# Kernel optimization log

Hardware: AMD Instinct MI355X
Metric: run time of the kernel (lower is better)

## Reference

```python
import jax, jax.numpy as jnp
import numpy as np

B, N, P = 8, 4096, 1024
P4 = P // 4
EPS = 1e-5


def _ln(x, g, b):
    mu = jnp.mean(x, axis=-1, keepdims=True)
    var = jnp.var(x, axis=-1, keepdims=True)
    return (x - mu) * jax.lax.rsqrt(var + EPS) * g + b


def setup_inputs() -> dict:
    key = jax.random.key(0)
    ks = jax.random.split(key, 16)
    s = lambda fan: 1.0 / np.sqrt(fan)
    return {
        "xyz": jax.random.normal(ks[0], (B, N, 3), jnp.float32),
        "x": jax.random.normal(ks[1], (B, N, P), jnp.float32),
        "ln1_g": jnp.ones((P,), jnp.float32),
        "ln1_b": jnp.zeros((P,), jnp.float32),
        "ln2_g": jnp.ones((P,), jnp.float32),
        "ln2_b": jnp.zeros((P,), jnp.float32),
        "qk_w": jax.random.normal(ks[2], (P4, P), jnp.float32) * s(P),   # shared q/k 1x1 conv, no bias
        "v_w": jax.random.normal(ks[3], (P, P), jnp.float32) * s(P),
        "v_b": jax.random.normal(ks[4], (P,), jnp.float32) * s(P),
        "t1_w": jax.random.normal(ks[5], (P, P4), jnp.float32) * s(P4),  # trans_conv
        "t1_b": jax.random.normal(ks[6], (P,), jnp.float32) * s(P4),
        "t2_w": jax.random.normal(ks[7], (P, P4), jnp.float32) * s(P4),  # trans_conv1
        "t2_b": jax.random.normal(ks[8], (P,), jnp.float32) * s(P4),
        "m1_w": jax.random.normal(ks[9], (P, P), jnp.float32) * s(P),
        "m1_b": jax.random.normal(ks[10], (P,), jnp.float32) * s(P),
        "m2_w": jax.random.normal(ks[11], (P, P), jnp.float32) * s(P),
        "m2_b": jax.random.normal(ks[12], (P,), jnp.float32) * s(P),
    }


def reference(xyz, x, ln1_g, ln1_b, ln2_g, ln2_b, qk_w, v_w, v_b,
              t1_w, t1_b, t2_w, t2_b, m1_w, m1_b, m2_w, m2_b):
    # xyz is accepted but unused, matching the torch module. Dropout = eval identity.
    res1 = x
    h = _ln(x, ln1_g, ln1_b)                                   # [B,N,P]
    # TransformerBlock_1 (1x1 convs on h^T [B,P,N] are just matmuls over P)
    x_q = jnp.einsum('op,bnp->bon', qk_w, h)                   # [B,P4,N]
    # k shares weights with q; x_k permuted is x_q transposed
    x_v = jnp.einsum('op,bnp->bno', v_w, h) + v_b              # [B,N,P]
    energy = jnp.einsum('bqn,bkn->bqk', x_q, x_q)              # [B,P4,P4]
    att = jnp.einsum('op,bpk->bok', t1_w, energy) + t1_b[:, None]   # [B,P,P4]
    att = jax.nn.gelu(att, approximate=False)
    att = jnp.einsum('op,bkp->bok', t2_w, att) + t2_b[:, None]      # [B,P,P]
    att = jax.nn.softmax(att, axis=-1)
    t_out = jnp.einsum('bnp,bpq->bnq', x_v, att)               # [B,N,P]
    x1 = t_out + res1
    h2 = _ln(x1, ln2_g, ln2_b)
    m = jax.nn.gelu(h2 @ m1_w.T + m1_b, approximate=False)
    m = m @ m2_w.T + m2_b
    return x1 + m
```

## Files before the change

### kernel.cpp

```cpp
#include <hip/hip_runtime.h>


typedef __attribute__((ext_vector_type(4))) float f32x4;
typedef __attribute__((ext_vector_type(8))) _Float16 h16x8;
typedef __attribute__((ext_vector_type(8))) unsigned short u16x8;
typedef __attribute__((ext_vector_type(4))) unsigned short u16x4;

__device__ __forceinline__ unsigned short f2h(float f) {
  _Float16 h = (_Float16)f;
  return __builtin_bit_cast(unsigned short, h);
}
__device__ __forceinline__ float h2f(unsigned short u) {
  return (float)__builtin_bit_cast(_Float16, u);
}
__device__ __forceinline__ unsigned split16(float f) {
  _Float16 h = (_Float16)f;
  _Float16 l = (_Float16)(f - (float)h);
  return (unsigned)__builtin_bit_cast(unsigned short, h) |
         ((unsigned)__builtin_bit_cast(unsigned short, l) << 16);
}
__device__ __forceinline__ float gelu_f(float x) {
  return 0.5f * x * (1.0f + erff(x * 0.70710678118654752f));
}
__device__ __forceinline__ void gload16(const void* g, void* l) {
  __builtin_amdgcn_global_load_lds(
      (const __attribute__((address_space(1))) unsigned int*)g,
      (__attribute__((address_space(3))) unsigned int*)l, 16, 0, 0);
}
#define FENCE() asm volatile("" ::: "memory")

__device__ __forceinline__ void xcd_swz(int& bx, int& by, int gx, int gy) {
  const int nwg = gx * gy;
  if ((nwg & 7) == 0 && nwg >= 16) {
    const int flat = bx + gx * by;
    const int chunk = nwg >> 3;
    const int nf = (flat & 7) * chunk + (flat >> 3);
    bx = nf % gx;
    by = nf / gx;
  }
}

__global__ __launch_bounds__(256)
void ln_kernel(const float* __restrict__ x, const float* __restrict__ g,
               const float* __restrict__ b, unsigned short* __restrict__ hi,
               unsigned short* __restrict__ lo, unsigned short* __restrict__ xh) {
  __shared__ float red[16];
  const size_t base = (size_t)blockIdx.x * 1024;
  const int t = threadIdx.x;
  f32x4 v = *(const f32x4*)&x[base + t * 4];
  float s = v[0] + v[1] + v[2] + v[3];
  float q = v[0] * v[0] + v[1] * v[1] + v[2] * v[2] + v[3] * v[3];
#pragma unroll
  for (int o = 32; o > 0; o >>= 1) { s += __shfl_down(s, o); q += __shfl_down(q, o); }
  const int w = t >> 6;
  if ((t & 63) == 0) { red[w] = s; red[8 + w] = q; }
  __syncthreads();
  s = (red[0] + red[1]) + (red[2] + red[3]);
  q = (red[8] + red[9]) + (red[10] + red[11]);
  const float mu = s * (1.0f / 1024.0f);
  const float var = q * (1.0f / 1024.0f) - mu * mu;
  const float is = rsqrtf(var + 1e-5f);
  f32x4 gg = *(const f32x4*)&g[t * 4];
  f32x4 bb = *(const f32x4*)&b[t * 4];
  u16x4 oh, ol, ox;
#pragma unroll
  for (int j = 0; j < 4; j++) {
    float y = (v[j] - mu) * is * gg[j] + bb[j];
    unsigned p = split16(y);
    oh[j] = (unsigned short)(p & 0xffffu);
    ol[j] = (unsigned short)(p >> 16);
    ox[j] = f2h(v[j]);
  }
  *(u16x4*)&hi[base + t * 4] = oh;
  if (lo) *(u16x4*)&lo[base + t * 4] = ol;
  if (xh) *(u16x4*)&xh[base + t * 4] = ox;
}

__global__ __launch_bounds__(256)
void stats16_kernel(const unsigned short* __restrict__ x16, float* __restrict__ muis) {
  __shared__ float red[16];
  const size_t base = (size_t)blockIdx.x * 1024;
  const int t = threadIdx.x;
  u16x4 raw = *(const u16x4*)&x16[base + t * 4];
  float v[4];
#pragma unroll
  for (int j = 0; j < 4; j++) v[j] = h2f(raw[j]);
  float s = v[0] + v[1] + v[2] + v[3];
  float q = v[0] * v[0] + v[1] * v[1] + v[2] * v[2] + v[3] * v[3];
#pragma unroll
  for (int o = 32; o > 0; o >>= 1) { s += __shfl_down(s, o); q += __shfl_down(q, o); }
  const int w = t >> 6;
  if ((t & 63) == 0) { red[w] = s; red[8 + w] = q; }
  __syncthreads();
  if (t == 0) {
    s = (red[0] + red[1]) + (red[2] + red[3]);
    q = (red[8] + red[9]) + (red[10] + red[11]);
    const float mu = s * (1.0f / 1024.0f);
    const float var = q * (1.0f / 1024.0f) - mu * mu;
    muis[blockIdx.x * 2] = mu;
    muis[blockIdx.x * 2 + 1] = rsqrtf(var + 1e-5f);
  }
}

__global__ __launch_bounds__(256)
void cvt_kernel(const float* __restrict__ in, unsigned short* __restrict__ hi,
                unsigned short* __restrict__ lo, int n4) {
  int i = blockIdx.x * 256 + threadIdx.x;
  if (i < n4) {
    f32x4 v = *(const f32x4*)&in[(size_t)i * 4];
    u16x4 oh, ol;
#pragma unroll
    for (int j = 0; j < 4; j++) {
      unsigned p = split16(v[j]);
      oh[j] = (unsigned short)(p & 0xffffu);
      ol[j] = (unsigned short)(p >> 16);
    }
    *(u16x4*)&hi[(size_t)i * 4] = oh;
    if (lo) *(u16x4*)&lo[(size_t)i * 4] = ol;
  }
}

__global__ __launch_bounds__(256)
void vwt_kernel(const float* __restrict__ vw, unsigned short* __restrict__ wvt) {
  __shared__ float T[64][65];
  const int bx = blockIdx.x, by = blockIdx.y;
  const int t = threadIdx.x;
  const int lr = t >> 6, lc = t & 63;
#pragma unroll
  for (int i = 0; i < 16; ++i) {
    const int row = i * 4 + lr;
    T[row][lc] = vw[(size_t)(by * 64 + row) * 1024 + bx * 64 + lc];
  }
  __syncthreads();
#pragma unroll
  for (int i = 0; i < 16; ++i) {
    const int row = i * 4 + lr;
    wvt[(size_t)(bx * 64 + row) * 1024 + by * 64 + lc] = f2h(T[lc][row]);
  }
}

__global__ __launch_bounds__(256)
void beff_kernel(const unsigned short* __restrict__ attT, const float* __restrict__ vb,
                 float* __restrict__ beff) {
  const int b = blockIdx.y;
  const int q = blockIdx.x * 4 + (threadIdx.x >> 6);
  const int l = threadIdx.x & 63;
  const unsigned short* row = attT + ((size_t)b * 1024 + q) * 1024;
  float s = 0.0f;
#pragma unroll
  for (int i = 0; i < 2; ++i) {
    u16x8 v = *(const u16x8*)&row[(i * 64 + l) * 8];
    f32x4 vb0 = *(const f32x4*)&vb[(i * 64 + l) * 8];
    f32x4 vb1 = *(const f32x4*)&vb[(i * 64 + l) * 8 + 4];
#pragma unroll
    for (int j = 0; j < 4; j++) s += h2f(v[j]) * vb0[j];
#pragma unroll
    for (int j = 0; j < 4; j++) s += h2f(v[j + 4]) * vb1[j];
  }
#pragma unroll
  for (int o = 32; o > 0; o >>= 1) s += __shfl_down(s, o);
  if (l == 0) beff[b * 1024 + q] = s;
}

template <int EPI>
__global__ __launch_bounds__(256)
void gemm_v(const unsigned short* __restrict__ Ain, const unsigned short* __restrict__ Bin,
            void* __restrict__ Cout, const float* __restrict__ bias,
            const unsigned short* __restrict__ res16In,
            int K, int lda, int ldb, int ldc,
            long long sA, long long sB, long long sC, long long sBias, long long sRes) {
  __shared__ short As[2][4096];
  __shared__ short Bs[2][4096];
  const int z = blockIdx.z;
  const unsigned short* A = Ain + (size_t)z * sA;
  const unsigned short* B = Bin + (size_t)z * sB;
  int bx = blockIdx.x, by = blockIdx.y;
  xcd_swz(bx, by, gridDim.x, gridDim.y);
  const int mBase = by * 128, nBase = bx * 128;
  const int t = threadIdx.x, w = t >> 6, l = t & 63;
  const int r16 = l & 15, kq = l >> 4;
  const int wr = (w >> 1) * 64, wc = (w & 1) * 64;
  f32x4 acc[4][4] = {};

  auto stage = [&](int buf, int k0) {
#pragma unroll
    for (int i = 0; i < 2; ++i) {
      const int c = i * 256 + t;
      const int row = c >> 2, cc = c & 3;
      const int gc = cc ^ ((row >> 1) & 3);
      short* la = &As[buf][(i * 256 + w * 64) * 8];
      short* lb = &Bs[buf][(i * 256 + w * 64) * 8];
      gload16(&A[(size_t)(mBase + row) * lda + k0 + gc * 8], la);
      gload16(&B[(size_t)(nBase + row) * ldb + k0 + gc * 8], lb);
    }
  };

  const int nt = K >> 5;
  stage(0, 0);
  if (nt > 1) stage(1, 32);
  for (int ts = 0; ts < nt; ++ts) {
    const int cur = ts & 1;
    if (ts + 1 < nt) { asm volatile("s_waitcnt vmcnt(4)" ::: "memory"); }
    else             { asm volatile("s_waitcnt vmcnt(0)" ::: "memory"); }
    __builtin_amdgcn_s_barrier();
    FENCE();
    h16x8 aF[4], bF[4];
#pragma unroll
    for (int mi = 0; mi < 4; mi++) {
      const int r = wr + mi * 16 + r16;
      aF[mi] = *(const h16x8*)&As[cur][r * 32 + (kq ^ ((r >> 1) & 3)) * 8];
    }
#pragma unroll
    for (int ni = 0; ni < 4; ni++) {
      const int r = wc + ni * 16 + r16;
      bF[ni] = *(const h16x8*)&Bs[cur][r * 32 + (kq ^ ((r >> 1) & 3)) * 8];
    }
    __builtin_amdgcn_s_setprio(1);
#pragma unroll
    for (int mi = 0; mi < 4; mi++)
#pragma unroll
      for (int ni = 0; ni < 4; ni++)
        acc[mi][ni] = __builtin_amdgcn_mfma_f32_16x16x32_f16(aF[mi], bF[ni], acc[mi][ni], 0, 0, 0);
    __builtin_amdgcn_s_setprio(0);
    FENCE();
    __builtin_amdgcn_s_barrier();
    FENCE();
    if (ts + 2 < nt) stage(cur, (ts + 2) * 32);
  }
  FENCE();

  unsigned short* C16 = (unsigned short*)Cout + (size_t)z * sC;
  float* C32 = (float*)Cout + (size_t)z * sC;
  const float* bp = (EPI == 1 || EPI == 3 || EPI == 8) ? bias + (size_t)z * sBias : nullptr;
  const unsigned short* rp = (EPI == 3 || EPI == 8) ? res16In + (size_t)z * sRes : nullptr;

  if constexpr (EPI == 1 || EPI == 4 || EPI == 8) {
    short* ep = ((w & 2) ? &Bs[0][0] : &As[0][0]) + (w & 1) * 4096;
#pragma unroll
    for (int mi = 0; mi < 4; mi++) {
#pragma unroll
      for (int ni = 0; ni < 4; ni++) {
        const int cl = nBase + wc + ni * 16 + r16;
        const float bcol = bp ? bp[cl] : 0.0f;
#pragma unroll
        for (int r = 0; r < 4; r++) {
          float v = acc[mi][ni][r] + bcol;
          if (EPI == 1) v = gelu_f(v);
          ep[(mi * 16 + kq * 4 + r) * 64 + ni * 16 + r16] = (short)f2h(v);
        }
      }
    }
#pragma unroll
    for (int j = 0; j < 8; j++) {
      const int f = j * 512 + l * 8;
      const int row = f >> 6, col = f & 63;
      u16x8 v8 = *(const u16x8*)&ep[f];
      const size_t gi = (size_t)(mBase + wr + row) * ldc + nBase + wc + col;
      if (EPI == 8) {
        u16x8 r8 = *(const u16x8*)&rp[gi];
#pragma unroll
        for (int q = 0; q < 8; q++) v8[q] = f2h(h2f(v8[q]) + h2f(r8[q]));
      }
      *(u16x8*)&C16[gi] = v8;
    }
  } else {
#pragma unroll
    for (int mi = 0; mi < 4; mi++) {
#pragma unroll
      for (int ni = 0; ni < 4; ni++) {
        const int cl = nBase + wc + ni * 16 + r16;
        const float bcol = bp[cl];
#pragma unroll
        for (int r = 0; r < 4; r++) {
          const int rw = mBase + wr + mi * 16 + kq * 4 + r;
          const size_t idx = (size_t)rw * ldc + cl;
          C32[idx] = acc[mi][ni][r] + bcol + h2f(rp[idx]);
        }
      }
    }
  }
}

__global__ __launch_bounds__(256)
void gemm_r(const unsigned short* __restrict__ Ain, const unsigned short* __restrict__ Bin,
            unsigned short* __restrict__ Cout, const float* __restrict__ bias,
            const unsigned short* __restrict__ resIn,
            int K, int lda, int ldb, int ldc,
            long long sA, long long sB, long long sC, long long sBias, long long sRes) {
  __shared__ short As[2][4096];
  __shared__ short Bs[2][4096];
  const int z = blockIdx.z;
  const unsigned short* A = Ain + (size_t)z * sA;
  const unsigned short* B = Bin + (size_t)z * sB;
  int bx = blockIdx.x, by = blockIdx.y;
  xcd_swz(bx, by, gridDim.x, gridDim.y);
  const int mBase = by * 128, nBase = bx * 128;
  const int t = threadIdx.x, w = t >> 6, l = t & 63;
  const int r16 = l & 15, kq = l >> 4;
  const int wr = (w >> 1) * 64, wc = (w & 1) * 64;
  f32x4 acc[4][4] = {};

  const int row0 = t >> 2, row1 = 64 + (t >> 2);
  const int cc0 = t & 3;
  const int gc0 = cc0 ^ ((row0 >> 1) & 3);
  const int gc1 = cc0 ^ ((row1 >> 1) & 3);

  u16x8 ra0, ra1, rb0, rb1;
  auto loadreg = [&](int k0) {
    ra0 = *(const u16x8*)&A[(size_t)(mBase + row0) * lda + k0 + gc0 * 8];
    rb0 = *(const u16x8*)&B[(size_t)(nBase + row0) * ldb + k0 + gc0 * 8];
    ra1 = *(const u16x8*)&A[(size_t)(mBase + row1) * lda + k0 + gc1 * 8];
    rb1 = *(const u16x8*)&B[(size_t)(nBase + row1) * ldb + k0 + gc1 * 8];
  };
  auto dswrite = [&](int buf) {
    *(u16x8*)&As[buf][t * 8] = ra0;
    *(u16x8*)&Bs[buf][t * 8] = rb0;
    *(u16x8*)&As[buf][(256 + t) * 8] = ra1;
    *(u16x8*)&Bs[buf][(256 + t) * 8] = rb1;
  };

  const int nt = K >> 5;
  loadreg(0);
  dswrite(0);
  if (nt > 1) loadreg(32);
  asm volatile("s_waitcnt lgkmcnt(0)" ::: "memory");
  __builtin_amdgcn_s_barrier();
  FENCE();
  for (int ts = 0; ts < nt; ++ts) {
    const int cur = ts & 1;
    h16x8 aF[4], bF[4];
#pragma unroll
    for (int mi = 0; mi < 4; mi++) {
      const int r = wr + mi * 16 + r16;
      aF[mi] = *(const h16x8*)&As[cur][r * 32 + (kq ^ ((r >> 1) & 3)) * 8];
    }
#pragma unroll
    for (int ni = 0; ni < 4; ni++) {
      const int r = wc + ni * 16 + r16;
      bF[ni] = *(const h16x8*)&Bs[cur][r * 32 + (kq ^ ((r >> 1) & 3)) * 8];
    }
    __builtin_amdgcn_s_setprio(1);
#pragma unroll
    for (int mi = 0; mi < 4; mi++)
#pragma unroll
      for (int ni = 0; ni < 4; ni++)
        acc[mi][ni] = __builtin_amdgcn_mfma_f32_16x16x32_f16(aF[mi], bF[ni], acc[mi][ni], 0, 0, 0);
    __builtin_amdgcn_s_setprio(0);
    FENCE();
    if (ts + 1 < nt) {
      __builtin_amdgcn_s_barrier();
      FENCE();
      dswrite((ts + 1) & 1);
      if (ts + 2 < nt) loadreg((ts + 2) * 32);
      asm volatile("s_waitcnt lgkmcnt(0)" ::: "memory");
      FENCE();
      __builtin_amdgcn_s_barrier();
      FENCE();
    }
  }
  FENCE();

  unsigned short* C16 = Cout + (size_t)z * sC;
  const float* bp = bias + (size_t)z * sBias;
  const unsigned short* rp = resIn + (size_t)z * sRes;
  short* ep = ((w & 2) ? &Bs[0][0] : &As[0][0]) + (w & 1) * 4096;
#pragma unroll
  for (int mi = 0; mi < 4; mi++) {
#pragma unroll
    for (int ni = 0; ni < 4; ni++) {
      const int cl = nBase + wc + ni * 16 + r16;
      const float bcol = bp[cl];
#pragma unroll
      for (int r = 0; r < 4; r++)
        ep[(mi * 16 + kq * 4 + r) * 64 + ni * 16 + r16] =
            (short)f2h(acc[mi][ni][r] + bcol);
    }
  }
#pragma unroll
  for (int j = 0; j < 8; j++) {
    const int f = j * 512 + l * 8;
    const int row = f >> 6, col = f & 63;
    u16x8 v8 = *(const u16x8*)&ep[f];
    const size_t gi = (size_t)(mBase + wr + row) * ldc + nBase + wc + col;
    u16x8 r8 = *(const u16x8*)&rp[gi];
#pragma unroll
    for (int q = 0; q < 8; q++) v8[q] = f2h(h2f(v8[q]) + h2f(r8[q]));
    *(u16x8*)&C16[gi] = v8;
  }
}

__global__ __launch_bounds__(256)
void gemm_m(const unsigned short* __restrict__ Ain, const unsigned short* __restrict__ Bin,
            const float* __restrict__ muis, const float* __restrict__ lng,
            const float* __restrict__ lnb, const float* __restrict__ bias,
            unsigned short* __restrict__ Cout, int K, int lda, int ldb, int ldc) {
  __shared__ short As[2][4096];
  __shared__ short Bs[2][4096];
  int bx = blockIdx.x, by = blockIdx.y;
  xcd_swz(bx, by, gridDim.x, gridDim.y);
  const int mBase = by * 128, nBase = bx * 128;
  const int t = threadIdx.x, w = t >> 6, l = t & 63;
  const int r16 = l & 15, kq = l >> 4;
  const int wr = (w >> 1) * 64, wc = (w & 1) * 64;
  f32x4 acc[4][4] = {};

  const int row0 = t >> 2, row1 = 64 + (t >> 2);
  const int cc0 = t & 3;
  const int gc0 = cc0 ^ ((row0 >> 1) & 3);
  const int gc1 = cc0 ^ ((row1 >> 1) & 3);
  const float mu0 = muis[(mBase + row0) * 2], is0 = muis[(mBase + row0) * 2 + 1];
  const float mu1 = muis[(mBase + row1) * 2], is1 = muis[(mBase + row1) * 2 + 1];

  u16x8 ra0, ra1, rb0, rb1;
  auto loadreg = [&](int k0) {
    ra0 = *(const u16x8*)&Ain[(size_t)(mBase + row0) * lda + k0 + gc0 * 8];
    rb0 = *(const u16x8*)&Bin[(size_t)(nBase + row0) * ldb + k0 + gc0 * 8];
    ra1 = *(const u16x8*)&Ain[(size_t)(mBase + row1) * lda + k0 + gc1 * 8];
    rb1 = *(const u16x8*)&Bin[(size_t)(nBase + row1) * ldb + k0 + gc1 * 8];
  };
  auto dswrite = [&](int buf, int k0) {
    {
      const int cb = k0 + gc0 * 8;
      f32x4 g0 = *(const f32x4*)&lng[cb], g1 = *(const f32x4*)&lng[cb + 4];
      f32x4 b0 = *(const f32x4*)&lnb[cb], b1 = *(const f32x4*)&lnb[cb + 4];
      u16x8 o;
#pragma unroll
      for (int j = 0; j < 4; j++) o[j] = f2h((h2f(ra0[j]) - mu0) * is0 * g0[j] + b0[j]);
#pragma unroll
      for (int j = 0; j < 4; j++) o[j + 4] = f2h((h2f(ra0[j + 4]) - mu0) * is0 * g1[j] + b1[j]);
      *(u16x8*)&As[buf][t * 8] = o;
      *(u16x8*)&Bs[buf][t * 8] = rb0;
    }
    {
      const int cb = k0 + gc1 * 8;
      f32x4 g0 = *(const f32x4*)&lng[cb], g1 = *(const f32x4*)&lng[cb + 4];
      f32x4 b0 = *(const f32x4*)&lnb[cb], b1 = *(const f32x4*)&lnb[cb + 4];
      u16x8 o;
#pragma unroll
      for (int j = 0; j < 4; j++) o[j] = f2h((h2f(ra1[j]) - mu1) * is1 * g0[j] + b0[j]);
#pragma unroll
      for (int j = 0; j < 4; j++) o[j + 4] = f2h((h2f(ra1[j + 4]) - mu1) * is1 * g1[j] + b1[j]);
      *(u16x8*)&As[buf][(256 + t) * 8] = o;
      *(u16x8*)&Bs[buf][(256 + t) * 8] = rb1;
    }
  };

  const int nt = K >> 5;
  loadreg(0);
  dswrite(0, 0);
  if (nt > 1) loadreg(32);
  asm volatile("s_waitcnt lgkmcnt(0)" ::: "memory");
  __builtin_amdgcn_s_barrier();
  FENCE();
  for (int ts = 0; ts < nt; ++ts) {
    const int cur = ts & 1;
    h16x8 aF[4], bF[4];
#pragma unroll
    for (int mi = 0; mi < 4; mi++) {
      const int r = wr + mi * 16 + r16;
      aF[mi] = *(const h16x8*)&As[cur][r * 32 + (kq ^ ((r >> 1) & 3)) * 8];
    }
#pragma unroll
    for (int ni = 0; ni < 4; ni++) {
      const int r = wc + ni * 16 + r16;
      bF[ni] = *(const h16x8*)&Bs[cur][r * 32 + (kq ^ ((r >> 1) & 3)) * 8];
    }
    __builtin_amdgcn_s_setprio(1);
#pragma unroll
    for (int mi = 0; mi < 4; mi++)
#pragma unroll
      for (int ni = 0; ni < 4; ni++)
        acc[mi][ni] = __builtin_amdgcn_mfma_f32_16x16x32_f16(aF[mi], bF[ni], acc[mi][ni], 0, 0, 0);
    __builtin_amdgcn_s_setprio(0);
    FENCE();
    if (ts + 1 < nt) {
      __builtin_amdgcn_s_barrier();
      FENCE();
      dswrite((ts + 1) & 1, (ts + 1) * 32);
      if (ts + 2 < nt) loadreg((ts + 2) * 32);
      asm volatile("s_waitcnt lgkmcnt(0)" ::: "memory");
      FENCE();
      __builtin_amdgcn_s_barrier();
      FENCE();
    }
  }
  FENCE();

  short* ep = ((w & 2) ? &Bs[0][0] : &As[0][0]) + (w & 1) * 4096;
#pragma unroll
  for (int mi = 0; mi < 4; mi++) {
#pragma unroll
    for (int ni = 0; ni < 4; ni++) {
      const int cl = nBase + wc + ni * 16 + r16;
      const float bcol = bias[cl];
#pragma unroll
      for (int r = 0; r < 4; r++)
        ep[(mi * 16 + kq * 4 + r) * 64 + ni * 16 + r16] =
            (short)f2h(gelu_f(acc[mi][ni][r] + bcol));
    }
  }
#pragma unroll
  for (int j = 0; j < 8; j++) {
    const int f = j * 512 + l * 8;
    const int row = f >> 6, col = f & 63;
    *(u16x8*)&Cout[(size_t)(mBase + wr + row) * ldc + nBase + wc + col] =
        *(const u16x8*)&ep[f];
  }
}

template <int EPI, int SWAP>
__global__ __launch_bounds__(256)
void gemm_s(const unsigned short* __restrict__ Ahi, const unsigned short* __restrict__ Alo,
            const unsigned short* __restrict__ Bhi, const unsigned short* __restrict__ Blo,
            void* __restrict__ Cout, unsigned short* __restrict__ Cout2,
            const float* __restrict__ bias,
            int K, int lda, int ldb, int ldc,
            long long sA, long long sB, long long sC, int splitK) {
  __shared__ short As[2][8192];
  __shared__ short Bs[2][8192];
  const int z = blockIdx.z;
  const int bi = z / splitK, sp = z % splitK;
  const int kLen = K / splitK, kStart = sp * kLen;
  const unsigned short* AH = Ahi + (size_t)bi * sA;
  const unsigned short* BH = Bhi + (size_t)bi * sB;
  const unsigned short* AL = Alo + (size_t)bi * sA;
  const unsigned short* BL = Blo + (size_t)bi * sB;
  int bx = blockIdx.x, by = blockIdx.y;
  xcd_swz(bx, by, gridDim.x, gridDim.y);
  const int mBase = (SWAP ? bx : by) * 128, nBase = (SWAP ? by : bx) * 128;
  const int t = threadIdx.x, w = t >> 6, l = t & 63;
  const int r16 = l & 15, kq = l >> 4;
  const int wr = (w >> 1) * 64, wc = (w & 1) * 64;
  f32x4 acc[4][4] = {};

  auto stage = [&](int buf, int k0) {
#pragma unroll
    for (int i = 0; i < 2; ++i) {
      const int c = i * 256 + t;
      const int row = c >> 2, cc = c & 3;
      const int gc = cc ^ ((row >> 1) & 3);
      const int cbase = i * 256 + w * 64;
      const size_t ga = (size_t)(mBase + row) * lda + k0 + gc * 8;
      const size_t gb = (size_t)(nBase + row) * ldb + k0 + gc * 8;
      gload16(&AH[ga], &As[buf][cbase * 8]);
      gload16(&AL[ga], &As[buf][4096 + cbase * 8]);
      gload16(&BH[gb], &Bs[buf][cbase * 8]);
      gload16(&BL[gb], &Bs[buf][4096 + cbase * 8]);
    }
  };

  const int nsteps = kLen >> 5;
  stage(0, kStart);
  if (nsteps > 1) stage(1, kStart + 32);
  for (int ts = 0; ts < nsteps; ++ts) {
    const int cur = ts & 1;
    if (ts + 1 < nsteps) { asm volatile("s_waitcnt vmcnt(8)" ::: "memory"); }
    else                 { asm volatile("s_waitcnt vmcnt(0)" ::: "memory"); }
    __builtin_amdgcn_s_barrier();
    FENCE();
    h16x8 aH[4], bH[4], aL[4], bL[4];
#pragma unroll
    for (int mi = 0; mi < 4; mi++) {
      const int r = wr + mi * 16 + r16;
      const int off = r * 32 + (kq ^ ((r >> 1) & 3)) * 8;
      aH[mi] = *(const h16x8*)&As[cur][off];
      aL[mi] = *(const h16x8*)&As[cur][4096 + off];
    }
#pragma unroll
    for (int ni = 0; ni < 4; ni++) {
      const int r = wc + ni * 16 + r16;
      const int off = r * 32 + (kq ^ ((r >> 1) & 3)) * 8;
      bH[ni] = *(const h16x8*)&Bs[cur][off];
      bL[ni] = *(const h16x8*)&Bs[cur][4096 + off];
    }
    __builtin_amdgcn_s_setprio(1);
#pragma unroll
    for (int mi = 0; mi < 4; mi++)
#pragma unroll
      for (int ni = 0; ni < 4; ni++) {
        acc[mi][ni] = __builtin_amdgcn_mfma_f32_16x16x32_f16(aH[mi], bH[ni], acc[mi][ni], 0, 0, 0);
        acc[mi][ni] = __builtin_amdgcn_mfma_f32_16x16x32_f16(aH[mi], bL[ni], acc[mi][ni], 0, 0, 0);
        acc[mi][ni] = __builtin_amdgcn_mfma_f32_16x16x32_f16(aL[mi], bH[ni], acc[mi][ni], 0, 0, 0);
      }
    __builtin_amdgcn_s_setprio(0);
    FENCE();
    __builtin_amdgcn_s_barrier();
    FENCE();
    if (ts + 2 < nsteps) stage(cur, kStart + (ts + 2) * 32);
  }
  FENCE();

  unsigned short* C16 = (unsigned short*)Cout + (size_t)z * sC;
  unsigned short* C16b = Cout2 ? Cout2 + (size_t)z * sC : nullptr;
  float* C32 = (float*)Cout + (size_t)z * sC;

  if constexpr (EPI == 4 || EPI == 6) {
    short* ep = &As[0][0] + w * 4096;
    unsigned pk[4][4][4];
#pragma unroll
    for (int mi = 0; mi < 4; mi++)
#pragma unroll
      for (int ni = 0; ni < 4; ni++)
#pragma unroll
        for (int r = 0; r < 4; r++) {
          float v = acc[mi][ni][r];
          if (EPI == 6) { v += bias[mBase + wr + mi * 16 + kq * 4 + r]; v = gelu_f(v); }
          pk[mi][ni][r] = split16(v);
        }
#pragma unroll
    for (int mi = 0; mi < 4; mi++)
#pragma unroll
      for (int ni = 0; ni < 4; ni++)
#pragma unroll
        for (int r = 0; r < 4; r++)
          ep[(mi * 16 + kq * 4 + r) * 64 + ni * 16 + r16] =
              (short)(pk[mi][ni][r] & 0xffffu);
#pragma unroll
    for (int j = 0; j < 8; j++) {
      const int f = j * 512 + l * 8;
      const int row = f >> 6, col = f & 63;
      *(u16x8*)&C16[(size_t)(mBase + wr + row) * ldc + nBase + wc + col] =
          *(const u16x8*)&ep[f];
    }
#pragma unroll
    for (int mi = 0; mi < 4; mi++)
#pragma unroll
      for (int ni = 0; ni < 4; ni++)
#pragma unroll
        for (int r = 0; r < 4; r++)
          ep[(mi * 16 + kq * 4 + r) * 64 + ni * 16 + r16] =
              (short)(pk[mi][ni][r] >> 16);
#pragma unroll
    for (int j = 0; j < 8; j++) {
      const int f = j * 512 + l * 8;
      const int row = f >> 6, col = f & 63;
      *(u16x8*)&C16b[(size_t)(mBase + wr + row) * ldc + nBase + wc + col] =
          *(const u16x8*)&ep[f];
    }
  } else {
#pragma unroll
    for (int mi = 0; mi < 4; mi++) {
#pragma unroll
      for (int ni = 0; ni < 4; ni++) {
        const int cl = nBase + wc + ni * 16 + r16;
#pragma unroll
        for (int r = 0; r < 4; r++) {
          const int rw = mBase + wr + mi * 16 + kq * 4 + r;
          float v = acc[mi][ni][r];
          if (EPI == 7) v += bias[rw];
          C32[(size_t)rw * ldc + cl] = v;
        }
      }
    }
  }
}

__global__ __launch_bounds__(256)
void ereduce_kernel(const float* __restrict__ part, unsigned short* __restrict__ ehi,
                    unsigned short* __restrict__ elo) {
  const size_t idx = (size_t)blockIdx.x * 256 + threadIdx.x;
  const size_t b = idx >> 16, i = idx & 65535;
  const float* p = part + b * (8ull * 65536) + i;
  float s0 = (p[0] + p[65536]) + (p[2 * 65536] + p[3 * 65536]);
  float s1 = (p[4 * 65536] + p[5 * 65536]) + (p[6 * 65536] + p[7 * 65536]);
  unsigned pk = split16(s0 + s1);
  ehi[idx] = (unsigned short)(pk & 0xffffu);
  elo[idx] = (unsigned short)(pk >> 16);
}

__global__ __launch_bounds__(256)
void smax_t_kernel(const float* __restrict__ a2, unsigned short* __restrict__ attT) {
  __shared__ float S[8][1028];
  __shared__ float inv[8];
  const int t = threadIdx.x;
  const int b = blockIdx.y;
  const int o0 = blockIdx.x * 8;
  const float* src = a2 + ((size_t)b * 1024 + o0) * 1024;
#pragma unroll
  for (int i = 0; i < 8; i++)
    *(f32x4*)&S[i][t * 4] = *(const f32x4*)&src[(size_t)i * 1024 + t * 4];
  __syncthreads();
  const int w = t >> 6, l = t & 63;
  for (int rr = 0; rr < 2; rr++) {
    const int r = w * 2 + rr;
    float m = -1e30f;
#pragma unroll
    for (int i = 0; i < 16; i++) m = fmaxf(m, S[r][l + i * 64]);
#pragma unroll
    for (int o = 32; o > 0; o >>= 1) m = fmaxf(m, __shfl_xor(m, o));
    float ssum = 0.0f;
#pragma unroll
    for (int i = 0; i < 16; i++) {
      float e = expf(S[r][l + i * 64] - m);
      S[r][l + i * 64] = e;
      ssum += e;
    }
#pragma unroll
    for (int o = 32; o > 0; o >>= 1) ssum += __shfl_xor(ssum, o);
    if (l == 0) inv[r] = 1.0f / ssum;
  }
  __syncthreads();
  float iv[8];
#pragma unroll
  for (int r = 0; r < 8; r++) iv[r] = inv[r];
#pragma unroll
  for (int i = 0; i < 4; i++) {
    const int k = i * 256 + t;
    u16x8 ov;
#pragma unroll
    for (int r = 0; r < 8; r++) ov[r] = f2h(S[r][k] * iv[r]);
    *(u16x8*)&attT[((size_t)b * 1024 + k) * 1024 + o0] = ov;
  }
}

extern "C" void kernel_launch(void* const* d_in, const int* in_sizes, int n_in,
                              void* d_out, int out_size, void* d_ws, size_t ws_size,
                              hipStream_t stream) {
  (void)in_sizes; (void)n_in; (void)out_size; (void)ws_size;
  const float* x     = (const float*)d_in[1];
  const float* ln1_g = (const float*)d_in[2];
  const float* ln1_b = (const float*)d_in[3];
  const float* ln2_g = (const float*)d_in[4];
  const float* ln2_b = (const float*)d_in[5];
  const float* qk_w  = (const float*)d_in[6];
  const float* v_w   = (const float*)d_in[7];
  const float* v_b   = (const float*)d_in[8];
  const float* t1_w  = (const float*)d_in[9];
  const float* t1_b  = (const float*)d_in[10];
  const float* t2_w  = (const float*)d_in[11];
  const float* t2_b  = (const float*)d_in[12];
  const float* m1_w  = (const float*)d_in[13];
  const float* m1_b  = (const float*)d_in[14];
  const float* m2_w  = (const float*)d_in[15];
  const float* m2_b  = (const float*)d_in[16];

  char* ws = (char*)d_ws;
  unsigned short* hhi  = (unsigned short*)(ws + 0);
  unsigned short* hlo  = (unsigned short*)(ws + 67108864);
  unsigned short* Qthi = (unsigned short*)(ws + 134217728);
  unsigned short* Qtlo = (unsigned short*)(ws + 150994944);
  float*          part = (float*)(ws + 167772160);
  unsigned short* Ehi  = (unsigned short*)(ws + 184549376);
  unsigned short* Elo  = (unsigned short*)(ws + 185597952);
  unsigned short* Ghi  = (unsigned short*)(ws + 186646528);
  unsigned short* Glo  = (unsigned short*)(ws + 190840832);
  float*          a2   = (float*)(ws + 195035136);
  unsigned short* attT = (unsigned short*)(ws + 228589568);
  unsigned short* WeT  = (unsigned short*)(ws + 245366784);
  float*          beff = (float*)(ws + 262144000);
  float*          muis = (float*)(ws + 262176768);
  unsigned short* xh   = (unsigned short*)(ws + 268435456);
  unsigned short* x1h  = (unsigned short*)(ws + 335544320);
  unsigned short* wqh  = (unsigned short*)(ws + 446693376);
  unsigned short* wql  = (unsigned short*)(ws + 447217664);
  unsigned short* wvt  = (unsigned short*)(ws + 447741952);
  unsigned short* wt1h = (unsigned short*)(ws + 449839104);
  unsigned short* wt1l = (unsigned short*)(ws + 450363392);
  unsigned short* wt2h = (unsigned short*)(ws + 450887680);
  unsigned short* wt2l = (unsigned short*)(ws + 451411968);
  unsigned short* wm1  = (unsigned short*)(ws + 451936256);
  unsigned short* wm2  = (unsigned short*)(ws + 454033408);
  unsigned short* gb = hlo;
  float* out = (float*)d_out;

  cvt_kernel<<<dim3(256),  dim3(256), 0, stream>>>(qk_w, wqh, wql, 65536);
  vwt_kernel<<<dim3(16, 16), dim3(256), 0, stream>>>(v_w, wvt);
  cvt_kernel<<<dim3(256),  dim3(256), 0, stream>>>(t1_w, wt1h, wt1l, 65536);
  cvt_kernel<<<dim3(256),  dim3(256), 0, stream>>>(t2_w, wt2h, wt2l, 65536);
  cvt_kernel<<<dim3(1024), dim3(256), 0, stream>>>(m1_w, wm1, nullptr, 262144);
  cvt_kernel<<<dim3(1024), dim3(256), 0, stream>>>(m2_w, wm2, nullptr, 262144);
  ln_kernel<<<dim3(32768), dim3(256), 0, stream>>>(x, ln1_g, ln1_b, hhi, hlo, xh);
  gemm_s<4, 1><<<dim3(2, 32, 8), dim3(256), 0, stream>>>(
      wqh, wql, hhi, hlo, Qthi, Qtlo, nullptr,
      1024, 1024, 1024, 4096, 0, 4194304, 1048576, 1);
  gemm_s<5, 0><<<dim3(2, 2, 64), dim3(256), 0, stream>>>(
      Qthi, Qtlo, Qthi, Qtlo, part, nullptr, nullptr,
      4096, 4096, 4096, 256, 1048576, 1048576, 65536, 8);
  ereduce_kernel<<<dim3(2048), dim3(256), 0, stream>>>(part, Ehi, Elo);
  gemm_s<6, 0><<<dim3(2, 8, 8), dim3(256), 0, stream>>>(
      wt1h, wt1l, Ehi, Elo, Ghi, Glo, t1_b,
      256, 256, 256, 256, 0, 65536, 262144, 1);
  gemm_s<7, 0><<<dim3(8, 8, 8), dim3(256), 0, stream>>>(
      wt2h, wt2l, Ghi, Glo, a2, nullptr, t2_b,
      256, 256, 256, 1024, 0, 262144, 1048576, 1);
  smax_t_kernel<<<dim3(128, 8), dim3(256), 0, stream>>>(a2, attT);
  gemm_v<4><<<dim3(8, 8, 8), dim3(256), 0, stream>>>(
      attT, wvt, WeT, nullptr, nullptr,
      1024, 1024, 1024, 1024, 1048576, 0, 1048576, 0, 0);
  beff_kernel<<<dim3(256, 8), dim3(256), 0, stream>>>(attT, v_b, beff);
  gemm_r<<<dim3(8, 32, 8), dim3(256), 0, stream>>>(
      hhi, WeT, x1h, beff, xh,
      1024, 1024, 1024, 1024, 4194304, 1048576, 4194304, 1024, 4194304);
  stats16_kernel<<<dim3(32768), dim3(256), 0, stream>>>(x1h, muis);
  gemm_m<<<dim3(8, 256, 1), dim3(256), 0, stream>>>(
      x1h, wm1, muis, ln2_g, ln2_b, m1_b, gb, 1024, 1024, 1024, 1024);
  gemm_v<3><<<dim3(8, 256, 1), dim3(256), 0, stream>>>(
      gb, wm2, out, m2_b, x1h, 1024, 1024, 1024, 1024, 0, 0, 0, 0, 0);
}
```

Measured before the change: 660.9 us.

## Fold LayerNorm2 into MLP1 weights and apply normalization in the GEMM epilogue

Rewrites LN2 followed by the m1 matmul algebraically. The weights are pre-scaled by gamma, and a per-column sum S and an effective bias (m1_b plus W·beta) are precomputed. The GEMM then consumes raw x1 half-precision values and applies is*(acc - mu*S) + b2 plus GELU in the epilogue. This removes the per-tile normalization arithmetic in the load path of the old gemm_m and lets it reuse the generic pipelined gemm_v kernel. The subtraction mu*S happens after fp16 accumulation of unnormalized x1, which may cost accuracy when the row mean is large.

```diff
diff --git a/kernel.cpp b/kernel.cpp
--- a/kernel.cpp
+++ b/kernel.cpp
@@ -121,6 +121,39 @@
 }
 
 __global__ __launch_bounds__(256)
+void m1prep_kernel(const float* __restrict__ m1w, const float* __restrict__ lng,
+                   const float* __restrict__ lnb, const float* __restrict__ m1b,
+                   unsigned short* __restrict__ wp, float* __restrict__ S,
+                   float* __restrict__ b2) {
+  __shared__ float red[16];
+  const int o = blockIdx.x;
+  const int t = threadIdx.x;
+  const float* row = m1w + (size_t)o * 1024;
+  f32x4 wv = *(const f32x4*)&row[t * 4];
+  f32x4 gv = *(const f32x4*)&lng[t * 4];
+  f32x4 bv = *(const f32x4*)&lnb[t * 4];
+  float s = 0.0f, d = 0.0f;
+  u16x4 ow;
+#pragma unroll
+  for (int j = 0; j < 4; j++) {
+    float wpj = wv[j] * gv[j];
+    ow[j] = f2h(wpj);
+    s += wpj;
+    d += wv[j] * bv[j];
+  }
+  *(u16x4*)&wp[(size_t)o * 1024 + t * 4] = ow;
+#pragma unroll
+  for (int off = 32; off > 0; off >>= 1) { s += __shfl_down(s, off); d += __shfl_down(d, off); }
+  const int w = t >> 6;
+  if ((t & 63) == 0) { red[w] = s; red[8 + w] = d; }
+  __syncthreads();
+  if (t == 0) {
+    S[o] = (red[0] + red[1]) + (red[2] + red[3]);
+    b2[o] = m1b[o] + (red[8] + red[9]) + (red[10] + red[11]);
+  }
+}
+
+__global__ __launch_bounds__(256)
 void vwt_kernel(const float* __restrict__ vw, unsigned short* __restrict__ wvt) {
   __shared__ float T[64][65];
   const int bx = blockIdx.x, by = blockIdx.y;
@@ -166,7 +199,8 @@
 __global__ __launch_bounds__(256)
 void gemm_v(const unsigned short* __restrict__ Ain, const unsigned short* __restrict__ Bin,
             void* __restrict__ Cout, const float* __restrict__ bias,
-            const unsigned short* __restrict__ res16In,
+            const unsigned short* __restrict__ res16In, const float* __restrict__ muis,
+            const float* __restrict__ Svec,
             int K, int lda, int ldb, int ldc,
             long long sA, long long sB, long long sC, long long sBias, long long sRes) {
   __shared__ short As[2][4096];
@@ -231,21 +265,35 @@
 
   unsigned short* C16 = (unsigned short*)Cout + (size_t)z * sC;
   float* C32 = (float*)Cout + (size_t)z * sC;
-  const float* bp = (EPI == 1 || EPI == 3 || EPI == 8) ? bias + (size_t)z * sBias : nullptr;
-  const unsigned short* rp = (EPI == 3 || EPI == 8) ? res16In + (size_t)z * sRes : nullptr;
-
-  if constexpr (EPI == 1 || EPI == 4 || EPI == 8) {
+  const float* bp = (EPI != 4) ? bias + (size_t)z * sBias : nullptr;
+  const unsigned short* rp = (EPI == 3) ? res16In + (size_t)z * sRes : nullptr;
+
+  if constexpr (EPI == 1 || EPI == 4 || EPI == 9) {
     short* ep = ((w & 2) ? &Bs[0][0] : &As[0][0]) + (w & 1) * 4096;
 #pragma unroll
     for (int mi = 0; mi < 4; mi++) {
+      float mu[4], is[4];
+      if (EPI == 9) {
+#pragma unroll
+        for (int r = 0; r < 4; r++) {
+          const int rw = mBase + wr + mi * 16 + kq * 4 + r;
+          mu[r] = muis[rw * 2];
+          is[r] = muis[rw * 2 + 1];
+        }
+      }
 #pragma unroll
       for (int ni = 0; ni < 4; ni++) {
         const int cl = nBase + wc + ni * 16 + r16;
         const float bcol = bp ? bp[cl] : 0.0f;
+        const float Scol = (EPI == 9) ? Svec[cl] : 0.0f;
 #pragma unroll
         for (int r = 0; r < 4; r++) {
-          float v = acc[mi][ni][r] + bcol;
-          if (EPI == 1) v = gelu_f(v);
+          float v;
+          if (EPI == 9) v = gelu_f(is[r] * (acc[mi][ni][r] - mu[r] * Scol) + bcol);
+          else {
+            v = acc[mi][ni][r] + bcol;
+            if (EPI == 1) v = gelu_f(v);
+          }
           ep[(mi * 16 + kq * 4 + r) * 64 + ni * 16 + r16] = (short)f2h(v);
         }
       }
@@ -254,14 +302,8 @@
     for (int j = 0; j < 8; j++) {
       const int f = j * 512 + l * 8;
       const int row = f >> 6, col = f & 63;
-      u16x8 v8 = *(const u16x8*)&ep[f];
       const size_t gi = (size_t)(mBase + wr + row) * ldc + nBase + wc + col;
-      if (EPI == 8) {
-        u16x8 r8 = *(const u16x8*)&rp[gi];
-#pragma unroll
-        for (int q = 0; q < 8; q++) v8[q] = f2h(h2f(v8[q]) + h2f(r8[q]));
-      }
-      *(u16x8*)&C16[gi] = v8;
+      *(u16x8*)&C16[gi] = *(const u16x8*)&ep[f];
     }
   } else {
 #pragma unroll
@@ -386,125 +428,6 @@
 #pragma unroll
     for (int q = 0; q < 8; q++) v8[q] = f2h(h2f(v8[q]) + h2f(r8[q]));
     *(u16x8*)&C16[gi] = v8;
-  }
-}
-
-__global__ __launch_bounds__(256)
-void gemm_m(const unsigned short* __restrict__ Ain, const unsigned short* __restrict__ Bin,
-            const float* __restrict__ muis, const float* __restrict__ lng,
-            const float* __restrict__ lnb, const float* __restrict__ bias,
-            unsigned short* __restrict__ Cout, int K, int lda, int ldb, int ldc) {
-  __shared__ short As[2][4096];
-  __shared__ short Bs[2][4096];
-  int bx = blockIdx.x, by = blockIdx.y;
-  xcd_swz(bx, by, gridDim.x, gridDim.y);
-  const int mBase = by * 128, nBase = bx * 128;
-  const int t = threadIdx.x, w = t >> 6, l = t & 63;
-  const int r16 = l & 15, kq = l >> 4;
-  const int wr = (w >> 1) * 64, wc = (w & 1) * 64;
-  f32x4 acc[4][4] = {};
-
-  const int row0 = t >> 2, row1 = 64 + (t >> 2);
-  const int cc0 = t & 3;
-  const int gc0 = cc0 ^ ((row0 >> 1) & 3);
-  const int gc1 = cc0 ^ ((row1 >> 1) & 3);
-  const float mu0 = muis[(mBase + row0) * 2], is0 = muis[(mBase + row0) * 2 + 1];
-  const float mu1 = muis[(mBase + row1) * 2], is1 = muis[(mBase + row1) * 2 + 1];
-
-  u16x8 ra0, ra1, rb0, rb1;
-  auto loadreg = [&](int k0) {
-    ra0 = *(const u16x8*)&Ain[(size_t)(mBase + row0) * lda + k0 + gc0 * 8];
-    rb0 = *(const u16x8*)&Bin[(size_t)(nBase + row0) * ldb + k0 + gc0 * 8];
-    ra1 = *(const u16x8*)&Ain[(size_t)(mBase + row1) * lda + k0 + gc1 * 8];
-    rb1 = *(const u16x8*)&Bin[(size_t)(nBase + row1) * ldb + k0 + gc1 * 8];
-  };
-  auto dswrite = [&](int buf, int k0) {
-    {
-      const int cb = k0 + gc0 * 8;
-      f32x4 g0 = *(const f32x4*)&lng[cb], g1 = *(const f32x4*)&lng[cb + 4];
-      f32x4 b0 = *(const f32x4*)&lnb[cb], b1 = *(const f32x4*)&lnb[cb + 4];
-      u16x8 o;
-#pragma unroll
-      for (int j = 0; j < 4; j++) o[j] = f2h((h2f(ra0[j]) - mu0) * is0 * g0[j] + b0[j]);
-#pragma unroll
-      for (int j = 0; j < 4; j++) o[j + 4] = f2h((h2f(ra0[j + 4]) - mu0) * is0 * g1[j] + b1[j]);
-      *(u16x8*)&As[buf][t * 8] = o;
-      *(u16x8*)&Bs[buf][t * 8] = rb0;
-    }
-    {
-      const int cb = k0 + gc1 * 8;
-      f32x4 g0 = *(const f32x4*)&lng[cb], g1 = *(const f32x4*)&lng[cb + 4];
-      f32x4 b0 = *(const f32x4*)&lnb[cb], b1 = *(const f32x4*)&lnb[cb + 4];
-      u16x8 o;
-#pragma unroll
-      for (int j = 0; j < 4; j++) o[j] = f2h((h2f(ra1[j]) - mu1) * is1 * g0[j] + b0[j]);
-#pragma unroll
-      for (int j = 0; j < 4; j++) o[j + 4] = f2h((h2f(ra1[j + 4]) - mu1) * is1 * g1[j] + b1[j]);
-      *(u16x8*)&As[buf][(256 + t) * 8] = o;
-      *(u16x8*)&Bs[buf][(256 + t) * 8] = rb1;
-    }
-  };
-
-  const int nt = K >> 5;
-  loadreg(0);
-  dswrite(0, 0);
-  if (nt > 1) loadreg(32);
-  asm volatile("s_waitcnt lgkmcnt(0)" ::: "memory");
-  __builtin_amdgcn_s_barrier();
-  FENCE();
-  for (int ts = 0; ts < nt; ++ts) {
-    const int cur = ts & 1;
-    h16x8 aF[4], bF[4];
-#pragma unroll
-    for (int mi = 0; mi < 4; mi++) {
-      const int r = wr + mi * 16 + r16;
-      aF[mi] = *(const h16x8*)&As[cur][r * 32 + (kq ^ ((r >> 1) & 3)) * 8];
-    }
-#pragma unroll
-    for (int ni = 0; ni < 4; ni++) {
-      const int r = wc + ni * 16 + r16;
-      bF[ni] = *(const h16x8*)&Bs[cur][r * 32 + (kq ^ ((r >> 1) & 3)) * 8];
-    }
-    __builtin_amdgcn_s_setprio(1);
-#pragma unroll
-    for (int mi = 0; mi < 4; mi++)
-#pragma unroll
-      for (int ni = 0; ni < 4; ni++)
-        acc[mi][ni] = __builtin_amdgcn_mfma_f32_16x16x32_f16(aF[mi], bF[ni], acc[mi][ni], 0, 0, 0);
-    __builtin_amdgcn_s_setprio(0);
-    FENCE();
-    if (ts + 1 < nt) {
-      __builtin_amdgcn_s_barrier();
-      FENCE();
-      dswrite((ts + 1) & 1, (ts + 1) * 32);
-      if (ts + 2 < nt) loadreg((ts + 2) * 32);
-      asm volatile("s_waitcnt lgkmcnt(0)" ::: "memory");
-      FENCE();
-      __builtin_amdgcn_s_barrier();
-      FENCE();
-    }
-  }
-  FENCE();
-
-  short* ep = ((w & 2) ? &Bs[0][0] : &As[0][0]) + (w & 1) * 4096;
-#pragma unroll
-  for (int mi = 0; mi < 4; mi++) {
-#pragma unroll
-    for (int ni = 0; ni < 4; ni++) {
-      const int cl = nBase + wc + ni * 16 + r16;
-      const float bcol = bias[cl];
-#pragma unroll
-      for (int r = 0; r < 4; r++)
-        ep[(mi * 16 + kq * 4 + r) * 64 + ni * 16 + r16] =
-            (short)f2h(gelu_f(acc[mi][ni][r] + bcol));
-    }
-  }
-#pragma unroll
-  for (int j = 0; j < 8; j++) {
-    const int f = j * 512 + l * 8;
-    const int row = f >> 6, col = f & 63;
-    *(u16x8*)&Cout[(size_t)(mBase + wr + row) * ldc + nBase + wc + col] =
-        *(const u16x8*)&ep[f];
   }
 }
 
@@ -749,6 +672,8 @@
   unsigned short* WeT  = (unsigned short*)(ws + 245366784);
   float*          beff = (float*)(ws + 262144000);
   float*          muis = (float*)(ws + 262176768);
+  float*          Svec = (float*)(ws + 262438912);
+  float*          b2   = (float*)(ws + 262443008);
   unsigned short* xh   = (unsigned short*)(ws + 268435456);
   unsigned short* x1h  = (unsigned short*)(ws + 335544320);
   unsigned short* wqh  = (unsigned short*)(ws + 446693376);
@@ -758,7 +683,7 @@
   unsigned short* wt1l = (unsigned short*)(ws + 450363392);
   unsigned short* wt2h = (unsigned short*)(ws + 450887680);
   unsigned short* wt2l = (unsigned short*)(ws + 451411968);
-  unsigned short* wm1  = (unsigned short*)(ws + 451936256);
+  unsigned short* wm1p = (unsigned short*)(ws + 451936256);
   unsigned short* wm2  = (unsigned short*)(ws + 454033408);
   unsigned short* gb = hlo;
   float* out = (float*)d_out;
@@ -767,7 +692,7 @@
   vwt_kernel<<<dim3(16, 16), dim3(256), 0, stream>>>(v_w, wvt);
   cvt_kernel<<<dim3(256),  dim3(256), 0, stream>>>(t1_w, wt1h, wt1l, 65536);
   cvt_kernel<<<dim3(256),  dim3(256), 0, stream>>>(t2_w, wt2h, wt2l, 65536);
-  cvt_kernel<<<dim3(1024), dim3(256), 0, stream>>>(m1_w, wm1, nullptr, 262144);
+  m1prep_kernel<<<dim3(1024), dim3(256), 0, stream>>>(m1_w, ln2_g, ln2_b, m1_b, wm1p, Svec, b2);
   cvt_kernel<<<dim3(1024), dim3(256), 0, stream>>>(m2_w, wm2, nullptr, 262144);
   ln_kernel<<<dim3(32768), dim3(256), 0, stream>>>(x, ln1_g, ln1_b, hhi, hlo, xh);
   gemm_s<4, 1><<<dim3(2, 32, 8), dim3(256), 0, stream>>>(
@@ -785,15 +710,17 @@
       256, 256, 256, 1024, 0, 262144, 1048576, 1);
   smax_t_kernel<<<dim3(128, 8), dim3(256), 0, stream>>>(a2, attT);
   gemm_v<4><<<dim3(8, 8, 8), dim3(256), 0, stream>>>(
-      attT, wvt, WeT, nullptr, nullptr,
+      attT, wvt, WeT, nullptr, nullptr, nullptr, nullptr,
       1024, 1024, 1024, 1024, 1048576, 0, 1048576, 0, 0);
   beff_kernel<<<dim3(256, 8), dim3(256), 0, stream>>>(attT, v_b, beff);
   gemm_r<<<dim3(8, 32, 8), dim3(256), 0, stream>>>(
       hhi, WeT, x1h, beff, xh,
       1024, 1024, 1024, 1024, 4194304, 1048576, 4194304, 1024, 4194304);
   stats16_kernel<<<dim3(32768), dim3(256), 0, stream>>>(x1h, muis);
-  gemm_m<<<dim3(8, 256, 1), dim3(256), 0, stream>>>(
-      x1h, wm1, muis, ln2_g, ln2_b, m1_b, gb, 1024, 1024, 1024, 1024);
+  gemm_v<9><<<dim3(8, 256, 1), dim3(256), 0, stream>>>(
+      x1h, wm1p, gb, b2, nullptr, muis, Svec,
+      1024, 1024, 1024, 1024, 0, 0, 0, 0, 0);
   gemm_v<3><<<dim3(8, 256, 1), dim3(256), 0, stream>>>(
-      gb, wm2, out, m2_b, x1h, 1024, 1024, 1024, 1024, 0, 0, 0, 0, 0);
-}
+      gb, wm2, out, m2_b, x1h, nullptr, nullptr,
+      1024, 1024, 1024, 1024, 0, 0, 0, 0, 0);
+}
```

After: 634.8 us. -4.0%, faster.
